# Kernel optimization log

Hardware: AMD Instinct MI355X
Metric: run time of the kernel (lower is better)

The kernel has to match this reference:

```python
import jax, jax.numpy as jnp
import numpy as np

C = 512
H = 8
P = 64
B = 4
N = 1024


def setup_inputs() -> dict:
    key = jax.random.key(0)
    ks = jax.random.split(key, 12)
    s = 0.02
    return {
        "tokens": jax.random.normal(ks[0], (B, N, C), dtype=jnp.float32),
        "pair_features": jax.random.normal(ks[1], (N, N, P), dtype=jnp.float32),
        "Wq": jax.random.normal(ks[2], (C, C), dtype=jnp.float32) * s,
        "bq": jnp.zeros((C,), dtype=jnp.float32),
        "Wk": jax.random.normal(ks[3], (C, C), dtype=jnp.float32) * s,
        "bk": jnp.zeros((C,), dtype=jnp.float32),
        "Wv": jax.random.normal(ks[4], (C, C), dtype=jnp.float32) * s,
        "bv": jnp.zeros((C,), dtype=jnp.float32),
        "Wo": jax.random.normal(ks[5], (C, C), dtype=jnp.float32) * s,
        "bo": jnp.zeros((C,), dtype=jnp.float32),
        "Wp": jax.random.normal(ks[6], (P, H), dtype=jnp.float32) * s,
    }


def reference(tokens, pair_features, Wq, bq, Wk, bk, Wv, bv, Wo, bo, Wp):
    b, n, c = tokens.shape
    h = H
    d = c // h
    scale = d ** -0.5
    # projections -> [b, h, n, d]
    q = (tokens @ Wq + bq).reshape(b, n, h, d).transpose(0, 2, 1, 3)
    k = (tokens @ Wk + bk).reshape(b, n, h, d).transpose(0, 2, 1, 3)
    v = (tokens @ Wv + bv).reshape(b, n, h, d).transpose(0, 2, 1, 3)
    # attention logits [b, h, n, n] with additive pair-derived bias [h, n, n]
    logits = jnp.einsum('bhnd,bhmd->bhnm', q, k) * scale
    pair_bias = jnp.einsum('nmp,ph->hnm', pair_features, Wp)
    logits = logits + pair_bias[None]
    attn = jax.nn.softmax(logits, axis=-1)  # dropout p=0.0 -> identity
    merged = jnp.einsum('bhnm,bhmd->bhnd', attn, v)
    merged = merged.transpose(0, 2, 1, 3).reshape(b, n, c)
    return merged @ Wo + bo
```

## Files before the change

### kernel.cpp

```cpp
#include <hip/hip_runtime.h>
#include <hip/hip_bf16.h>
#include <stdint.h>
#include <stddef.h>

typedef __bf16 bf16x8 __attribute__((ext_vector_type(8)));
typedef __bf16 bf16x4 __attribute__((ext_vector_type(4)));
typedef float  f32x4  __attribute__((ext_vector_type(4)));
typedef uint32_t __attribute__((address_space(3))) lds_u32;
typedef uint32_t __attribute__((address_space(1))) glob_u32;

#define QKV_BLOCKS 384
#define PAIR_BLOCKS 2048
#define NSPLIT 2
#define NITER  8
#define LOG2E 1.4426950408889634f

__global__ __launch_bounds__(256) void k1_kernel(
    const float* __restrict__ tokens, const float* __restrict__ pf,
    const float* __restrict__ Wq, const float* __restrict__ Wk,
    const float* __restrict__ Wv, const float* __restrict__ Wp,
    const float* __restrict__ bq, const float* __restrict__ bk,
    const float* __restrict__ bv,
    __bf16* __restrict__ qb, __bf16* __restrict__ kb, __bf16* __restrict__ vtb,
    __bf16* __restrict__ pbb) {
  __shared__ __bf16 As[128][40];
  __shared__ __bf16 Bs[128][40];
  __shared__ float ftile[32][133];
  int bx = blockIdx.x, tid = threadIdx.x;
  if (bx < QKV_BLOCKS) {
    const float qscale = 0.125f * LOG2E;
    int nb = bx % 12, mb = bx / 12;
    int m0 = mb * 128, n0 = nb * 128;
    int sel = n0 >> 9, cloc = n0 & 511;
    const float* W = sel == 0 ? Wq : sel == 1 ? Wk : Wv;
    int wave = tid >> 6, lane = tid & 63;
    int wm = (wave >> 1) * 64, wn = (wave & 1) * 64;
    int lg = lane >> 4, lr = lane & 15;
    f32x4 acc[4][4];
#pragma unroll
    for (int i = 0; i < 4; ++i)
#pragma unroll
      for (int j = 0; j < 4; ++j) acc[i][j] = (f32x4){0.f, 0.f, 0.f, 0.f};

    for (int k0 = 0; k0 < 512; k0 += 32) {
      __syncthreads();
#pragma unroll
      for (int i = 0; i < 2; ++i) {
        int cid = tid + i * 256;
        int row = cid >> 2, c8 = (cid & 3) * 8;
        const float* src = &tokens[(size_t)(m0 + row) * 512 + k0 + c8];
        f32x4 f0 = *(const f32x4*)src, f1 = *(const f32x4*)(src + 4);
        bf16x8 v;
#pragma unroll
        for (int u = 0; u < 4; ++u) { v[u] = (__bf16)f0[u]; v[u + 4] = (__bf16)f1[u]; }
        *(bf16x8*)&As[row][c8] = v;
      }
#pragma unroll
      for (int i = 0; i < 2; ++i) {
        int cid = tid + i * 256;
        int kk = cid >> 4, n8 = (cid & 15) * 8;
        const float* src = &W[(size_t)(k0 + kk) * 512 + cloc + n8];
        *(f32x4*)&ftile[kk][n8] = *(const f32x4*)src;
        *(f32x4*)&ftile[kk][n8 + 4] = *(const f32x4*)(src + 4);
      }
      __syncthreads();
#pragma unroll
      for (int i = 0; i < 2; ++i) {
        int cid = tid + i * 256;
        int n = cid >> 2, kk8 = (cid & 3) * 8;
        bf16x8 v;
#pragma unroll
        for (int u = 0; u < 8; ++u) v[u] = (__bf16)ftile[kk8 + u][n];
        *(bf16x8*)&Bs[n][kk8] = v;
      }
      __syncthreads();
      bf16x8 af[4], bfr[4];
#pragma unroll
      for (int i = 0; i < 4; ++i) {
        af[i]  = *(const bf16x8*)&As[wm + i * 16 + lr][lg * 8];
        bfr[i] = *(const bf16x8*)&Bs[wn + i * 16 + lr][lg * 8];
      }
#pragma unroll
      for (int i = 0; i < 4; ++i)
#pragma unroll
        for (int j = 0; j < 4; ++j)
          acc[i][j] = __builtin_amdgcn_mfma_f32_16x16x32_bf16(af[i], bfr[j], acc[i][j], 0, 0, 0);
    }
#pragma unroll
    for (int i = 0; i < 4; ++i)
#pragma unroll
      for (int j = 0; j < 4; ++j) {
        int grow0 = m0 + wm + i * 16 + lg * 4;
        int gcol = n0 + wn + j * 16 + lr;
        int gsel = gcol >> 9, c = gcol & 511;
        int hh = c >> 6, dd = c & 63;
        int b = grow0 >> 10, n = grow0 & 1023;
        if (gsel == 2) {
          float bias = bv[c];
          bf16x4 pack;
#pragma unroll
          for (int r = 0; r < 4; ++r) pack[r] = (__bf16)(acc[i][j][r] + bias);
          *(bf16x4*)&vtb[(((size_t)(b * 8 + hh)) * 64 + dd) * 1024 + n] = pack;
        } else if (gsel == 0) {
          float bias = bq[c];
#pragma unroll
          for (int r = 0; r < 4; ++r)
            qb[(((size_t)(b * 8 + hh)) * 1024 + n + r) * 64 + dd] = (__bf16)((acc[i][j][r] + bias) * qscale);
        } else {
          float bias = bk[c];
#pragma unroll
          for (int r = 0; r < 4; ++r)
            kb[(((size_t)(b * 8 + hh)) * 1024 + n + r) * 64 + dd] = (__bf16)(acc[i][j][r] + bias);
        }
      }
  } else {
    int pb = bx - QKV_BLOCKS;
    int wave = tid >> 6, lane = tid & 63;
    int lg = lane >> 4, lr = lane & 15;
    bf16x8 whi[2], wlo[2];
#pragma unroll
    for (int s = 0; s < 2; ++s)
#pragma unroll
      for (int j = 0; j < 8; ++j) {
        int p = s * 32 + lg * 8 + j;
        float w = (lr < 8) ? Wp[p * 8 + lr] : 0.f;
        __bf16 h = (__bf16)w;
        whi[s][j] = h;
        wlo[s][j] = (__bf16)(w - (float)h);
      }
    int wbase = pb * 512 + wave * 128;
#pragma unroll 2
    for (int t = 0; t < 8; ++t) {
      int rowt = wbase + t * 16;
      const float* rp = pf + (size_t)(rowt + lr) * 64;
      f32x4 raw[2][2];
#pragma unroll
      for (int s = 0; s < 2; ++s) {
        raw[s][0] = *(const f32x4*)&rp[s * 32 + lg * 8];
        raw[s][1] = *(const f32x4*)&rp[s * 32 + lg * 8 + 4];
      }
      bf16x8 ahi[2], alo[2];
#pragma unroll
      for (int s = 0; s < 2; ++s)
#pragma unroll
        for (int j = 0; j < 8; ++j) {
          float x = raw[s][j >> 2][j & 3];
          __bf16 h = (__bf16)x;
          ahi[s][j] = h;
          alo[s][j] = (__bf16)(x - (float)h);
        }
      f32x4 acc = {0.f, 0.f, 0.f, 0.f};
#pragma unroll
      for (int s = 0; s < 2; ++s) {
        acc = __builtin_amdgcn_mfma_f32_16x16x32_bf16(ahi[s], whi[s], acc, 0, 0, 0);
        acc = __builtin_amdgcn_mfma_f32_16x16x32_bf16(ahi[s], wlo[s], acc, 0, 0, 0);
        acc = __builtin_amdgcn_mfma_f32_16x16x32_bf16(alo[s], whi[s], acc, 0, 0, 0);
      }
      if (lr < 8) {
        bf16x4 pk;
#pragma unroll
        for (int r = 0; r < 4; ++r) pk[r] = (__bf16)(acc[r] * LOG2E);
        *(bf16x4*)&pbb[((size_t)lr << 20) + rowt + lg * 4] = pk;
      }
    }
  }
}

__device__ __forceinline__ bf16x8 swz_read(const __bf16* buf, int r, int k) {
  int chunk = (r << 3) | (k ^ (r & 7));
  return *(const bf16x8*)&buf[chunk * 8];
}

__global__ __launch_bounds__(256) void flash_kernel(const __bf16* __restrict__ qg,
                                                    const __bf16* __restrict__ kg,
                                                    const __bf16* __restrict__ vtg,
                                                    const __bf16* __restrict__ pbg,
                                                    float* __restrict__ po,
                                                    float2* __restrict__ ml) {
  __shared__ __align__(16) __bf16 kvs[2][2][64 * 64];
  __shared__ __bf16 pls[4][16][72];
  int bh = blockIdx.y, z = blockIdx.z, h = bh & 7;
  int q0 = blockIdx.x * 64;
  int tid = threadIdx.x, wave = tid >> 6, lane = tid & 63;
  int lg = lane >> 4, lr = lane & 15;
  const __bf16* qp = qg + (size_t)bh * 65536;
  const __bf16* kp = kg + (size_t)bh * 65536;
  const __bf16* vp = vtg + (size_t)bh * 65536;
  const __bf16* pbh = pbg + ((size_t)h << 20);
  int qw0 = q0 + wave * 16;
  int kb0 = z * NITER;

  auto stage = [&](int buf, int kb2) {
#pragma unroll
    for (int p = 0; p < 2; ++p) {
      int c = p * 256 + wave * 64 + lane;
      int r = c >> 3, kk = c & 7;
      int g = (c & ~7) | (kk ^ (r & 7));
      const __bf16* gk = kp + (size_t)kb2 * 4096 + g * 8;
      const __bf16* gv = vp + (size_t)(g >> 3) * 1024 + kb2 * 64 + (g & 7) * 8;
      __builtin_amdgcn_global_load_lds((const glob_u32*)gk,
          (lds_u32*)&kvs[buf][0][(size_t)(p * 256 + wave * 64) * 8], 16, 0, 0);
      __builtin_amdgcn_global_load_lds((const glob_u32*)gv,
          (lds_u32*)&kvs[buf][1][(size_t)(p * 256 + wave * 64) * 8], 16, 0, 0);
    }
  };

  bf16x8 qf[2];
#pragma unroll
  for (int c = 0; c < 2; ++c)
    qf[c] = *(const bf16x8*)&qp[(size_t)(qw0 + lr) * 64 + c * 32 + lg * 8];

  float mrow = -1e30f, lrow = 0.f;
  f32x4 of[4] = {};

  stage(0, kb0);
  __syncthreads();

#pragma unroll
  for (int t = 0; t < NITER; ++t) {
    int kb2 = kb0 + t;
    if (t + 1 < NITER) stage((t + 1) & 1, kb2 + 1);
    const __bf16* kbuf = &kvs[t & 1][0][0];
    const __bf16* vbuf = &kvs[t & 1][1][0];

    bf16x8 kf[4][2];
#pragma unroll
    for (int n = 0; n < 4; ++n)
#pragma unroll
      for (int c = 0; c < 2; ++c)
        kf[n][c] = swz_read(kbuf, n * 16 + lr, c * 4 + lg);

    f32x4 sv[4];
#pragma unroll
    for (int n = 0; n < 4; ++n) {
      bf16x4 bias = *(const bf16x4*)&pbh[(size_t)(qw0 + lr) * 1024 + kb2 * 64 + n * 16 + lg * 4];
      f32x4 cb;
#pragma unroll
      for (int r = 0; r < 4; ++r) cb[r] = (float)bias[r];
      cb = __builtin_amdgcn_mfma_f32_16x16x32_bf16(kf[n][0], qf[0], cb, 0, 0, 0);
      cb = __builtin_amdgcn_mfma_f32_16x16x32_bf16(kf[n][1], qf[1], cb, 0, 0, 0);
      sv[n] = cb;
    }

    float tm = -1e30f;
#pragma unroll
    for (int n = 0; n < 4; ++n)
#pragma unroll
      for (int r = 0; r < 4; ++r) tm = fmaxf(tm, sv[n][r]);
    tm = fmaxf(tm, __shfl_xor(tm, 16));
    tm = fmaxf(tm, __shfl_xor(tm, 32));
    float newm = fmaxf(mrow, tm);
    float fs = exp2f(mrow - newm);
    mrow = newm;
    float rs = 0.f;
#pragma unroll
    for (int n = 0; n < 4; ++n)
#pragma unroll
      for (int r = 0; r < 4; ++r) {
        float p = exp2f(sv[n][r] - newm);
        sv[n][r] = p;
        rs += p;
      }
    rs += __shfl_xor(rs, 16);
    rs += __shfl_xor(rs, 32);
    lrow = lrow * fs + rs;

#pragma unroll
    for (int n = 0; n < 4; ++n) {
      bf16x4 pk;
#pragma unroll
      for (int r = 0; r < 4; ++r) pk[r] = (__bf16)sv[n][r];
      *(bf16x4*)&pls[wave][lr][n * 16 + lg * 4] = pk;
    }

#pragma unroll
    for (int r = 0; r < 4; ++r) {
      float fsq = __shfl(fs, (lane & 48) | (lg * 4 + r));
#pragma unroll
      for (int dn = 0; dn < 4; ++dn) of[dn][r] *= fsq;
    }

    bf16x8 pa[2];
#pragma unroll
    for (int c = 0; c < 2; ++c)
      pa[c] = *(const bf16x8*)&pls[wave][lr][c * 32 + lg * 8];
    bf16x8 vf[4][2];
#pragma unroll
    for (int dn = 0; dn < 4; ++dn)
#pragma unroll
      for (int c = 0; c < 2; ++c)
        vf[dn][c] = swz_read(vbuf, dn * 16 + lr, c * 4 + lg);
#pragma unroll
    for (int dn = 0; dn < 4; ++dn) {
      of[dn] = __builtin_amdgcn_mfma_f32_16x16x32_bf16(pa[0], vf[dn][0], of[dn], 0, 0, 0);
      of[dn] = __builtin_amdgcn_mfma_f32_16x16x32_bf16(pa[1], vf[dn][1], of[dn], 0, 0, 0);
    }
    __syncthreads();
  }

  if (lg == 0)
    ml[(size_t)z * 32768 + bh * 1024 + qw0 + lr] = make_float2(mrow, lrow);
#pragma unroll
  for (int r = 0; r < 4; ++r) {
    int q = qw0 + lg * 4 + r;
#pragma unroll
    for (int dn = 0; dn < 4; ++dn)
      po[((size_t)z * 32768 + bh * 1024 + q) * 64 + dn * 16 + lr] = of[dn][r];
  }
}

__global__ __launch_bounds__(256) void combine_kernel(const float* __restrict__ po,
                                                      const float2* __restrict__ ml,
                                                      __bf16* __restrict__ merged) {
  int e = blockIdx.x * 256 + threadIdx.x;
  int row = e >> 5, d2 = (e & 31) * 2;
  int bh = row >> 10, q = row & 1023, b = bh >> 3, h = bh & 7;
  float2 s[NSPLIT];
  float M = -1e30f;
#pragma unroll
  for (int zz = 0; zz < NSPLIT; ++zz) {
    s[zz] = ml[(size_t)zz * 32768 + row];
    M = fmaxf(M, s[zz].x);
  }
  float L = 0.f, ox = 0.f, oy = 0.f;
#pragma unroll
  for (int zz = 0; zz < NSPLIT; ++zz) {
    float w = exp2f(s[zz].x - M);
    L += w * s[zz].y;
    float2 p = *(const float2*)&po[((size_t)zz * 32768 + row) * 64 + d2];
    ox += w * p.x;
    oy += w * p.y;
  }
  float inv = 1.f / L;
  __bf16 pr[2] = {(__bf16)(ox * inv), (__bf16)(oy * inv)};
  *(uint32_t*)&merged[((size_t)(b * 1024 + q)) * 512 + h * 64 + d2] = *(uint32_t*)pr;
}

__global__ __launch_bounds__(256) void out_gemm_kernel(const __bf16* __restrict__ A,
                                                       const float* __restrict__ Wo,
                                                       const float* __restrict__ bo,
                                                       float* __restrict__ out) {
  __shared__ __bf16 As[128][40];
  __shared__ __bf16 Bs[128][40];
  __shared__ float ftile[32][133];
  int m0 = blockIdx.y * 128, n0 = blockIdx.x * 128;
  int tid = threadIdx.x, wave = tid >> 6, lane = tid & 63;
  int wm = (wave >> 1) * 64, wn = (wave & 1) * 64, lg = lane >> 4, lr = lane & 15;
  f32x4 acc[4][4];
#pragma unroll
  for (int i = 0; i < 4; ++i)
#pragma unroll
    for (int j = 0; j < 4; ++j) acc[i][j] = (f32x4){0.f, 0.f, 0.f, 0.f};

  for (int k0 = 0; k0 < 512; k0 += 32) {
    __syncthreads();
#pragma unroll
    for (int i = 0; i < 2; ++i) {
      int cid = tid + i * 256;
      int row = cid >> 2, c8 = (cid & 3) * 8;
      *(bf16x8*)&As[row][c8] = *(const bf16x8*)&A[(size_t)(m0 + row) * 512 + k0 + c8];
    }
#pragma unroll
    for (int i = 0; i < 2; ++i) {
      int cid = tid + i * 256;
      int kk = cid >> 4, n8 = (cid & 15) * 8;
      const float* src = &Wo[(size_t)(k0 + kk) * 512 + n0 + n8];
      *(f32x4*)&ftile[kk][n8] = *(const f32x4*)src;
      *(f32x4*)&ftile[kk][n8 + 4] = *(const f32x4*)(src + 4);
    }
    __syncthreads();
#pragma unroll
    for (int i = 0; i < 2; ++i) {
      int cid = tid + i * 256;
      int n = cid >> 2, kk8 = (cid & 3) * 8;
      bf16x8 v;
#pragma unroll
      for (int u = 0; u < 8; ++u) v[u] = (__bf16)ftile[kk8 + u][n];
      *(bf16x8*)&Bs[n][kk8] = v;
    }
    __syncthreads();
    bf16x8 af[4], bfr[4];
#pragma unroll
    for (int i = 0; i < 4; ++i) {
      af[i]  = *(const bf16x8*)&As[wm + i * 16 + lr][lg * 8];
      bfr[i] = *(const bf16x8*)&Bs[wn + i * 16 + lr][lg * 8];
    }
#pragma unroll
    for (int i = 0; i < 4; ++i)
#pragma unroll
      for (int j = 0; j < 4; ++j)
        acc[i][j] = __builtin_amdgcn_mfma_f32_16x16x32_bf16(af[i], bfr[j], acc[i][j], 0, 0, 0);
  }
#pragma unroll
  for (int i = 0; i < 4; ++i)
#pragma unroll
    for (int j = 0; j < 4; ++j)
#pragma unroll
      for (int r = 0; r < 4; ++r) {
        int grow = m0 + wm + i * 16 + lg * 4 + r;
        int gcol = n0 + wn + j * 16 + lr;
        out[(size_t)grow * 512 + gcol] = acc[i][j][r] + bo[gcol];
      }
}

extern "C" void kernel_launch(void* const* d_in, const int* in_sizes, int n_in,
                              void* d_out, int out_size, void* d_ws, size_t ws_size,
                              hipStream_t stream) {
  const float* tokens = (const float*)d_in[0];
  const float* pf     = (const float*)d_in[1];
  const float* Wq     = (const float*)d_in[2];
  const float* bq     = (const float*)d_in[3];
  const float* Wk     = (const float*)d_in[4];
  const float* bk     = (const float*)d_in[5];
  const float* Wv     = (const float*)d_in[6];
  const float* bv     = (const float*)d_in[7];
  const float* Wo     = (const float*)d_in[8];
  const float* bo     = (const float*)d_in[9];
  const float* Wp     = (const float*)d_in[10];
  float* out = (float*)d_out;

  char* ws = (char*)d_ws;
  size_t off = 0;
  auto alloc = [&](size_t bytes) { char* p = ws + off; off += (bytes + 255) & ~(size_t)255; return p; };
  __bf16* qb     = (__bf16*)alloc((size_t)32 * 1024 * 64 * 2);
  __bf16* kb     = (__bf16*)alloc((size_t)32 * 1024 * 64 * 2);
  __bf16* vtb    = (__bf16*)alloc((size_t)32 * 64 * 1024 * 2);
  __bf16* pbb    = (__bf16*)alloc((size_t)8 * 1024 * 1024 * 2);
  __bf16* merged = (__bf16*)alloc((size_t)4096 * 512 * 2);
  float*  po     = (float*)alloc((size_t)NSPLIT * 32 * 1024 * 64 * 4);
  float2* ml     = (float2*)alloc((size_t)NSPLIT * 32 * 1024 * 8);

  k1_kernel<<<QKV_BLOCKS + PAIR_BLOCKS, 256, 0, stream>>>(
      tokens, pf, Wq, Wk, Wv, Wp, bq, bk, bv, qb, kb, vtb, pbb);
  flash_kernel<<<dim3(16, 32, NSPLIT), 256, 0, stream>>>(qb, kb, vtb, pbb, po, ml);
  combine_kernel<<<4096, 256, 0, stream>>>(po, ml, merged);
  out_gemm_kernel<<<dim3(4, 32), 256, 0, stream>>>(merged, Wo, bo, out);
}
```

Baseline: 138.9 us.

## Coalesce pair-feature loads via LDS staging and drop split-bf16 MFMA passes

The pair-bias branch now loads pair_features with fully coalesced contiguous float4 reads, converts them to bf16 and stages them through a swizzled, double-buffered per-wave LDS region before reading MFMA fragments. It also removes the hi/lo bf16 split, cutting each 16-row tile from six MFMAs to two. Shared memory is unioned into one raw buffer so both branches fit. The gain is less global-load inefficiency and less ALU/MFMA work, at the cost of lower precision in the pair bias and no explicit barrier between the LDS writes and reads within a wave.

```diff
diff --git a/kernel.cpp b/kernel.cpp
--- a/kernel.cpp
+++ b/kernel.cpp
@@ -23,11 +23,12 @@
     const float* __restrict__ bv,
     __bf16* __restrict__ qb, __bf16* __restrict__ kb, __bf16* __restrict__ vtb,
     __bf16* __restrict__ pbb) {
-  __shared__ __bf16 As[128][40];
-  __shared__ __bf16 Bs[128][40];
-  __shared__ float ftile[32][133];
+  __shared__ __align__(16) char smem_raw[37504];
   int bx = blockIdx.x, tid = threadIdx.x;
   if (bx < QKV_BLOCKS) {
+    __bf16 (*As)[40] = (__bf16(*)[40])smem_raw;
+    __bf16 (*Bs)[40] = (__bf16(*)[40])(smem_raw + 10240);
+    float (*ftile)[133] = (float(*)[133])(smem_raw + 20480);
     const float qscale = 0.125f * LOG2E;
     int nb = bx % 12, mb = bx / 12;
     int m0 = mb * 128, n0 = nb * 128;
@@ -117,45 +118,45 @@
     int pb = bx - QKV_BLOCKS;
     int wave = tid >> 6, lane = tid & 63;
     int lg = lane >> 4, lr = lane & 15;
-    bf16x8 whi[2], wlo[2];
+    bf16x8 wfrag[2];
 #pragma unroll
     for (int s = 0; s < 2; ++s)
 #pragma unroll
       for (int j = 0; j < 8; ++j) {
         int p = s * 32 + lg * 8 + j;
-        float w = (lr < 8) ? Wp[p * 8 + lr] : 0.f;
-        __bf16 h = (__bf16)w;
-        whi[s][j] = h;
-        wlo[s][j] = (__bf16)(w - (float)h);
-      }
+        wfrag[s][j] = (lr < 8) ? (__bf16)Wp[p * 8 + lr] : (__bf16)0.f;
+      }
+    char* psbase = smem_raw + wave * 4096;
     int wbase = pb * 512 + wave * 128;
+    int wrow_lo = lane >> 4;
+    int wcol = lane & 15;
 #pragma unroll 2
-    for (int t = 0; t < 8; ++t) {
-      int rowt = wbase + t * 16;
-      const float* rp = pf + (size_t)(rowt + lr) * 64;
-      f32x4 raw[2][2];
+    for (int it = 0; it < 8; ++it) {
+      int rowt = wbase + it * 16;
+      const float* base = pf + (size_t)rowt * 64;
+      f32x4 v[4];
+#pragma unroll
+      for (int j = 0; j < 4; ++j)
+        v[j] = *(const f32x4*)(base + j * 256 + lane * 4);
+      char* ps = psbase + (it & 1) * 2048;
+#pragma unroll
+      for (int j = 0; j < 4; ++j) {
+        int jr = j * 4 + wrow_lo;
+        bf16x4 b;
+#pragma unroll
+        for (int u = 0; u < 4; ++u) b[u] = (__bf16)v[j][u];
+        int cbyte = ((((wcol >> 1) ^ (jr & 7)) << 4) | ((wcol & 1) << 3));
+        *(bf16x4*)(ps + jr * 128 + cbyte) = b;
+      }
+      bf16x8 af[2];
 #pragma unroll
       for (int s = 0; s < 2; ++s) {
-        raw[s][0] = *(const f32x4*)&rp[s * 32 + lg * 8];
-        raw[s][1] = *(const f32x4*)&rp[s * 32 + lg * 8 + 4];
-      }
-      bf16x8 ahi[2], alo[2];
-#pragma unroll
-      for (int s = 0; s < 2; ++s)
-#pragma unroll
-        for (int j = 0; j < 8; ++j) {
-          float x = raw[s][j >> 2][j & 3];
-          __bf16 h = (__bf16)x;
-          ahi[s][j] = h;
-          alo[s][j] = (__bf16)(x - (float)h);
-        }
+        int cb = ((s * 4 + lg) ^ (lr & 7)) << 4;
+        af[s] = *(const bf16x8*)(ps + lr * 128 + cb);
+      }
       f32x4 acc = {0.f, 0.f, 0.f, 0.f};
-#pragma unroll
-      for (int s = 0; s < 2; ++s) {
-        acc = __builtin_amdgcn_mfma_f32_16x16x32_bf16(ahi[s], whi[s], acc, 0, 0, 0);
-        acc = __builtin_amdgcn_mfma_f32_16x16x32_bf16(ahi[s], wlo[s], acc, 0, 0, 0);
-        acc = __builtin_amdgcn_mfma_f32_16x16x32_bf16(alo[s], whi[s], acc, 0, 0, 0);
-      }
+      acc = __builtin_amdgcn_mfma_f32_16x16x32_bf16(af[0], wfrag[0], acc, 0, 0, 0);
+      acc = __builtin_amdgcn_mfma_f32_16x16x32_bf16(af[1], wfrag[1], acc, 0, 0, 0);
       if (lr < 8) {
         bf16x4 pk;
 #pragma unroll
```

New measurement: 137.9 us. About the same (-0.8%).
